# Optimization experiments

Measured on AMD Instinct MI355X. Metric: run time of the kernel, lower is better.

Reference implementation:

```python
import jax, jax.numpy as jnp
import numpy as np

HIDDEN = 4096
N_HEADS = 32
N_KV_HEADS = 8
HEAD_DIM = HIDDEN // N_HEADS  # 128
ROPE_THETA = 10000.0


def rotate_half(x):
    x1, x2 = jnp.split(x, 2, axis=-1)
    return jnp.concatenate((-x2, x1), axis=-1)


def rope_cos_sin(seq_len, dim, theta, dtype):
    inv_freq = 1.0 / (theta ** (jnp.arange(0, dim, 2, dtype=jnp.float32) / dim))
    t = jnp.arange(seq_len, dtype=jnp.float32)
    freqs = jnp.outer(t, inv_freq)               # [S, D/2]
    emb = jnp.concatenate((freqs, freqs), axis=-1)  # [S, D]
    return jnp.cos(emb).astype(dtype), jnp.sin(emb).astype(dtype)


def setup_inputs() -> dict:
    key = jax.random.key(0)
    k0, k1, k2, k3, k4 = jax.random.split(key, 5)
    B, S = 1, 2048
    std = 1.0 / np.sqrt(HIDDEN)
    return {
        "hidden_states": jax.random.normal(k0, (B, S, HIDDEN), dtype=jnp.float32),
        "wq": jax.random.normal(k1, (N_HEADS * HEAD_DIM, HIDDEN), dtype=jnp.float32) * std,
        "wk": jax.random.normal(k2, (N_KV_HEADS * HEAD_DIM, HIDDEN), dtype=jnp.float32) * std,
        "wv": jax.random.normal(k3, (N_KV_HEADS * HEAD_DIM, HIDDEN), dtype=jnp.float32) * std,
        "wo": jax.random.normal(k4, (HIDDEN, N_HEADS * HEAD_DIM), dtype=jnp.float32) * std,
    }


def reference(hidden_states, wq, wk, wv, wo):
    B, S, _ = hidden_states.shape
    dtype = hidden_states.dtype
    G = N_HEADS // N_KV_HEADS  # query groups per kv head

    # projections (torch Linear: x @ W.T)
    q = (hidden_states @ wq.T).reshape(B, S, N_HEADS, HEAD_DIM).transpose(0, 2, 1, 3)      # [B,H,S,D]
    k = (hidden_states @ wk.T).reshape(B, S, N_KV_HEADS, HEAD_DIM).transpose(0, 2, 1, 3)   # [B,Hkv,S,D]
    v = (hidden_states @ wv.T).reshape(B, S, N_KV_HEADS, HEAD_DIM).transpose(0, 2, 1, 3)   # [B,Hkv,S,D]

    cos, sin = rope_cos_sin(S, HEAD_DIM, ROPE_THETA, dtype)  # [S,D]
    cos = cos[None, None]  # [1,1,S,D]
    sin = sin[None, None]
    q = q * cos + rotate_half(q) * sin
    k = k * cos + rotate_half(k) * sin

    # GQA: group query heads with their kv head (equivalent to repeat_interleave on kv)
    qg = q.reshape(B, N_KV_HEADS, G, S, HEAD_DIM)
    scale = 1.0 / np.sqrt(HEAD_DIM)
    scores = jnp.einsum("bkgsd,bktd->bkgst", qg, k) * scale  # [B,Hkv,G,S,S]

    causal = jnp.tril(jnp.ones((S, S), dtype=bool))
    scores = jnp.where(causal, scores, -jnp.inf)
    probs = jax.nn.softmax(scores.astype(jnp.float32), axis=-1).astype(dtype)

    out = jnp.einsum("bkgst,bktd->bkgsd", probs, v)  # [B,Hkv,G,S,D]
    out = out.reshape(B, N_HEADS, S, HEAD_DIM).transpose(0, 2, 1, 3).reshape(B, S, N_HEADS * HEAD_DIM)
    return out @ wo.T
```

## Files before the change

kernel.cpp:

```cpp
#include <hip/hip_runtime.h>
#include <hip/hip_bf16.h>


typedef _Float16 half4_t __attribute__((ext_vector_type(4)));
typedef _Float16 half8_t __attribute__((ext_vector_type(8)));
typedef float f32x4 __attribute__((ext_vector_type(4)));

#define S_LEN 2048
#define HID 4096
#define NH 32
#define NKV 8

__device__ __forceinline__ void gload_lds16(const void* g, void* l) {
  __builtin_amdgcn_global_load_lds((const __attribute__((address_space(1))) void*)g,
                                   (__attribute__((address_space(3))) void*)l, 16, 0, 0);
}

__global__ __launch_bounds__(256) void cvt_f32_f16(const float* __restrict__ src,
                                                   _Float16* __restrict__ dst, int n4) {
  int i = blockIdx.x * 256 + threadIdx.x;
  if (i >= n4) return;
  f32x4 v = *(const f32x4*)(src + (size_t)i * 4);
  half4_t h = {(_Float16)v[0], (_Float16)v[1], (_Float16)v[2], (_Float16)v[3]};
  *(half4_t*)(dst + (size_t)i * 4) = h;
}

__global__ __launch_bounds__(256) void cvt_qkv(const float* __restrict__ wq,
                                               const float* __restrict__ wk,
                                               const float* __restrict__ wv,
                                               _Float16* __restrict__ dst, int n4) {
  int i = blockIdx.x * 256 + threadIdx.x;
  if (i >= n4) return;
  size_t e = (size_t)i * 4;
  const float* src;
  size_t off;
  if (e < (size_t)4096 * 4096)      { src = wq; off = e; }
  else if (e < (size_t)5120 * 4096) { src = wk; off = e - (size_t)4096 * 4096; }
  else                              { src = wv; off = e - (size_t)5120 * 4096; }
  f32x4 v = *(const f32x4*)(src + off);
  half4_t h = {(_Float16)v[0], (_Float16)v[1], (_Float16)v[2], (_Float16)v[3]};
  *(half4_t*)(dst + e) = h;
}

__global__ __launch_bounds__(256) void rope_table_kernel(float* __restrict__ cost,
                                                         float* __restrict__ sint) {
  int i = blockIdx.x * 256 + threadIdx.x;
  int d = i & 63;
  int s = i >> 6;
  float inv = exp2f(-(float)d * (13.287712379549449f / 64.0f));
  float f = (float)s * inv;
  cost[i] = cosf(f);
  sint[i] = sinf(f);
}

__global__ __launch_bounds__(256) void rope_apply_q(_Float16* __restrict__ X,
                                                    const float* __restrict__ cost,
                                                    const float* __restrict__ sint) {
  int idx = blockIdx.x * 256 + threadIdx.x;
  int g = idx & 15;
  int tmp = idx >> 4;
  int h = tmp % NH;
  int s = tmp / NH;
  int d0 = g * 4;
  size_t base = (size_t)s * HID + h * 128 + d0;
  half4_t x1 = *(half4_t*)(X + base);
  half4_t x2 = *(half4_t*)(X + base + 64);
  const float* cp = cost + s * 64 + d0;
  const float* sp = sint + s * 64 + d0;
  half4_t y1, y2;
#pragma unroll
  for (int j = 0; j < 4; ++j) {
    float c = cp[j], sn = sp[j];
    float a = (float)x1[j], b = (float)x2[j];
    y1[j] = (_Float16)(a * c - b * sn);
    y2[j] = (_Float16)(b * c + a * sn);
  }
  *(half4_t*)(X + base) = y1;
  *(half4_t*)(X + base + 64) = y2;
}

__global__ __launch_bounds__(256) void rope_k2_inplace(_Float16* __restrict__ K2,
                                                       const float* __restrict__ cost,
                                                       const float* __restrict__ sint) {
  int idx = blockIdx.x * 256 + threadIdx.x;
  int g = idx & 15;
  int tmp = idx >> 4;
  int h = tmp % NKV;
  int s = tmp / NKV;
  int d0 = g * 4;
  size_t tb = (size_t)h * (S_LEN * 128) + (size_t)(s >> 4) * 2048 + (size_t)(s & 15) * 8;
  size_t a1 = tb + (size_t)(d0 >> 3) * 128 + (d0 & 7);
  size_t a2 = a1 + 1024;
  half4_t x1 = *(half4_t*)(K2 + a1);
  half4_t x2 = *(half4_t*)(K2 + a2);
  const float* cp = cost + s * 64 + d0;
  const float* sp = sint + s * 64 + d0;
  half4_t y1, y2;
#pragma unroll
  for (int j = 0; j < 4; ++j) {
    float c = cp[j], sn = sp[j];
    float a = (float)x1[j], b = (float)x2[j];
    y1[j] = (_Float16)(a * c - b * sn);
    y2[j] = (_Float16)(b * c + a * sn);
  }
  *(half4_t*)(K2 + a1) = y1;
  *(half4_t*)(K2 + a2) = y2;
}

template <int MODE>
__global__ __launch_bounds__(256) void gemmT(const _Float16* __restrict__ A,
                                             const _Float16* __restrict__ W,
                                             void* __restrict__ out,
                                             _Float16* __restrict__ K2,
                                             _Float16* __restrict__ V2) {
  const int id = blockIdx.x;
  const int xcd = id & 7, slot = id >> 3;
  const int c = (MODE == 0) ? (xcd * 6 + (slot >> 4)) : (xcd * 4 + (slot >> 4));
  const int m0 = (slot & 15) * 128;
  const int col0 = c * 128;
  __shared__ __align__(16) _Float16 As[3][128 * 32];
  __shared__ __align__(16) _Float16 Bs[3][128 * 32];
  const int t = threadIdx.x, w = t >> 6, l = t & 63, lr = l & 15, lg = l >> 4;
  const int wm = (w >> 1) * 64, wn = (w & 1) * 64;
  const int srow = l >> 2;
  const int scolS = (((l & 3) ^ ((l >> 3) & 3))) * 8;
  const int rc = (lr >> 1) & 3;
  const _Float16* ap = A + (size_t)m0 * 4096 + scolS;
  const _Float16* bp = W + (size_t)col0 * 4096 + scolS;

  f32x4 acc[4][4] = {};

#define STAGE(buf_, kb_)                                              \
  _Pragma("unroll") for (int it = 0; it < 2; ++it) {                  \
    const int ci = it * 4 + w;                                        \
    const int r = ci * 16 + srow;                                     \
    gload_lds16(ap + (size_t)r * 4096 + (kb_), &As[buf_][ci * 512]);  \
    gload_lds16(bp + (size_t)r * 4096 + (kb_), &Bs[buf_][ci * 512]);  \
  }

  STAGE(0, 0)
  STAGE(1, 32)

  for (int k = 0; k < 128; ++k) {
    const int kb2 = (k + 2) * 32;
    const int buf = k % 3;
    __builtin_amdgcn_s_barrier();
    __builtin_amdgcn_sched_barrier(0);
    if (kb2 < 4096) {
      STAGE((k + 2) % 3, kb2)
      asm volatile("s_waitcnt vmcnt(4)" ::: "memory");
    } else {
      asm volatile("s_waitcnt vmcnt(0)" ::: "memory");
    }
    __builtin_amdgcn_sched_barrier(0);
    __builtin_amdgcn_s_barrier();
    half8_t af[4], bf[4];
#pragma unroll
    for (int mi = 0; mi < 4; ++mi)
      af[mi] = *(const half8_t*)&As[buf][(wm + mi * 16 + lr) * 32 + (lg ^ rc) * 8];
#pragma unroll
    for (int ni = 0; ni < 4; ++ni)
      bf[ni] = *(const half8_t*)&Bs[buf][(wn + ni * 16 + lr) * 32 + (lg ^ rc) * 8];
#pragma unroll
    for (int mi = 0; mi < 4; ++mi)
#pragma unroll
      for (int ni = 0; ni < 4; ++ni)
        acc[mi][ni] = __builtin_amdgcn_mfma_f32_16x16x32_f16(af[mi], bf[ni], acc[mi][ni], 0, 0, 0);
  }
#undef STAGE

#pragma unroll
  for (int mi = 0; mi < 4; ++mi) {
#pragma unroll
    for (int ni = 0; ni < 4; ++ni) {
      const int row = m0 + wm + mi * 16 + lg * 4;
      const int col = col0 + wn + ni * 16 + lr;
      if (MODE == 1) {
#pragma unroll
        for (int i = 0; i < 4; ++i)
          ((float*)out)[(size_t)(row + i) * 4096 + col] = acc[mi][ni][i];
      } else {
        if (col < 4096) {
#pragma unroll
          for (int i = 0; i < 4; ++i)
            ((_Float16*)out)[(size_t)(row + i) * 4096 + col] = (_Float16)acc[mi][ni][i];
        } else if (col < 5120) {
          const int cl = col - 4096;
          const int h = cl >> 7, d = cl & 127;
          const size_t kk = (size_t)h * (S_LEN * 128) + (size_t)(row >> 4) * 2048 +
                            (size_t)(d >> 3) * 128 + (d & 7);
#pragma unroll
          for (int i = 0; i < 4; ++i)
            K2[kk + ((row + i) & 15) * 8] = (_Float16)acc[mi][ni][i];
        } else {
          const int cl = col - 5120;
          half4_t o;
#pragma unroll
          for (int i = 0; i < 4; ++i) o[i] = (_Float16)acc[mi][ni][i];
          *(half4_t*)(V2 + (size_t)(cl >> 7) * (S_LEN * 128) + (size_t)(row >> 4) * 2048 +
                      (size_t)(cl & 127) * 16 + (row & 15)) = o;
        }
      }
    }
  }
}

__global__ __launch_bounds__(256) void attn_kernel(const _Float16* __restrict__ Q,
                                                   const _Float16* __restrict__ K2,
                                                   const _Float16* __restrict__ V2,
                                                   _Float16* __restrict__ Op,
                                                   float* __restrict__ Md) {
  const int bid = blockIdx.x;
  const int hk = bid & 7;
  const int split = (bid >> 3) & 1;
  const int qt = 63 - (bid >> 4);
  const int w = threadIdx.x >> 6;
  const int h = hk * 4 + w;
  const int l = threadIdx.x & 63;
  const int lr = l & 15;
  const int lg = l >> 4;
  const float scale = 0.08838834764831845f;
  const float LOG2E = 1.4426950408889634f;
  const float NEG = -1.0e30f;

  const int half_steps = qt + 1;
  const int kt0 = split * half_steps;
  const int kt1 = kt0 + half_steps;

  int sq[2];
  half8_t qf[2][4];
#pragma unroll
  for (int qc = 0; qc < 2; ++qc) {
    sq[qc] = qt * 32 + qc * 16 + lr;
#pragma unroll
    for (int c = 0; c < 4; ++c)
      qf[qc][c] = *(const half8_t*)(Q + (size_t)sq[qc] * HID + h * 128 + c * 32 + lg * 8);
  }
  const _Float16* Kb = K2 + (size_t)hk * (S_LEN * 128);
  const _Float16* Vb = V2 + (size_t)hk * (S_LEN * 128);

  f32x4 acc[8][2] = {};
  float m[2] = {NEG, NEG};
  float den[2] = {0.f, 0.f};

  half8_t kfn[4];
#pragma unroll
  for (int c = 0; c < 4; ++c)
    kfn[c] = *(const half8_t*)(Kb + (size_t)kt0 * 2048 + (c * 4 + lg) * 128 + lr * 8);

  for (int kt = kt0; kt < kt1; ++kt) {
    half8_t kf[4];
#pragma unroll
    for (int c = 0; c < 4; ++c) kf[c] = kfn[c];
    if (kt + 1 < kt1) {
#pragma unroll
      for (int c = 0; c < 4; ++c)
        kfn[c] = *(const half8_t*)(Kb + (size_t)(kt + 1) * 2048 + (c * 4 + lg) * 128 + lr * 8);
    }
    f32x4 s0 = {0.f, 0.f, 0.f, 0.f}, s1 = {0.f, 0.f, 0.f, 0.f};
    __builtin_amdgcn_s_setprio(1);
#pragma unroll
    for (int c = 0; c < 4; ++c) {
      s0 = __builtin_amdgcn_mfma_f32_16x16x32_f16(kf[c], qf[0][c], s0, 0, 0, 0);
      s1 = __builtin_amdgcn_mfma_f32_16x16x32_f16(kf[c], qf[1][c], s1, 0, 0, 0);
    }
    __builtin_amdgcn_s_setprio(0);
    half4_t vf[8];
#pragma unroll
    for (int dc = 0; dc < 8; ++dc)
      vf[dc] = *(const half4_t*)(Vb + (size_t)kt * 2048 + (dc * 16 + lr) * 16 + lg * 4);
    const int kbase = kt * 16 + lg * 4;
    float sc[2][4];
#pragma unroll
    for (int i = 0; i < 4; ++i) {
      sc[0][i] = s0[i] * scale;
      sc[1][i] = s1[i] * scale;
    }
    if (kt >= 2 * qt) {
#pragma unroll
      for (int qc = 0; qc < 2; ++qc)
#pragma unroll
        for (int i = 0; i < 4; ++i)
          if (kbase + i > sq[qc]) sc[qc][i] = NEG;
    }
    half4_t pf[2];
#pragma unroll
    for (int qc = 0; qc < 2; ++qc) {
      float mx = fmaxf(fmaxf(sc[qc][0], sc[qc][1]), fmaxf(sc[qc][2], sc[qc][3]));
      mx = fmaxf(mx, __shfl_xor(mx, 16));
      mx = fmaxf(mx, __shfl_xor(mx, 32));
      if (!__all(mx - m[qc] <= 8.0f)) {
        float mn = fmaxf(m[qc], mx);
        float corr = exp2f((m[qc] - mn) * LOG2E);
        den[qc] *= corr;
#pragma unroll
        for (int dc = 0; dc < 8; ++dc)
#pragma unroll
          for (int i = 0; i < 4; ++i) acc[dc][qc][i] *= corr;
        m[qc] = mn;
      }
      float ps = 0.f, p[4];
#pragma unroll
      for (int i = 0; i < 4; ++i) {
        p[i] = exp2f((sc[qc][i] - m[qc]) * LOG2E);
        ps += p[i];
      }
      ps += __shfl_xor(ps, 16);
      ps += __shfl_xor(ps, 32);
      den[qc] += ps;
      pf[qc] = (half4_t){(_Float16)p[0], (_Float16)p[1], (_Float16)p[2], (_Float16)p[3]};
    }
    __builtin_amdgcn_s_setprio(1);
#pragma unroll
    for (int dc = 0; dc < 8; ++dc) {
      acc[dc][0] = __builtin_amdgcn_mfma_f32_16x16x16f16(vf[dc], pf[0], acc[dc][0], 0, 0, 0);
      acc[dc][1] = __builtin_amdgcn_mfma_f32_16x16x16f16(vf[dc], pf[1], acc[dc][1], 0, 0, 0);
    }
    __builtin_amdgcn_s_setprio(0);
  }

  _Float16* Os = Op + (size_t)split * S_LEN * HID;
#pragma unroll
  for (int qc = 0; qc < 2; ++qc) {
    float inv = den[qc] > 0.f ? 1.0f / den[qc] : 0.f;
#pragma unroll
    for (int dc = 0; dc < 8; ++dc) {
      half4_t o;
#pragma unroll
      for (int i = 0; i < 4; ++i) o[i] = (_Float16)(acc[dc][qc][i] * inv);
      *(half4_t*)(Os + (size_t)sq[qc] * HID + h * 128 + dc * 16 + lg * 4) = o;
    }
    if (lg == 0) {
      int mdix = ((split * S_LEN + sq[qc]) * NH + h) * 2;
      Md[mdix] = m[qc];
      Md[mdix + 1] = den[qc];
    }
  }
}

__global__ __launch_bounds__(256) void attn_combine(const _Float16* __restrict__ Op,
                                                    const float* __restrict__ Md,
                                                    _Float16* __restrict__ O) {
  const float LOG2E = 1.4426950408889634f;
  int idx = blockIdx.x * 256 + threadIdx.x;
  int dd = (idx & 15) * 8;
  int h = (idx >> 4) & 31;
  int s = idx >> 9;
  int base = (s * NH + h) * 2;
  float m0 = Md[base], den0 = Md[base + 1];
  float m1 = Md[S_LEN * NH * 2 + base], den1 = Md[S_LEN * NH * 2 + base + 1];
  float M = fmaxf(m0, m1);
  float w0 = den0 * exp2f((m0 - M) * LOG2E);
  float w1 = den1 * exp2f((m1 - M) * LOG2E);
  float r = 1.0f / (w0 + w1);
  w0 *= r;
  w1 *= r;
  size_t off = (size_t)s * HID + h * 128 + dd;
  half8_t a = *(const half8_t*)(Op + off);
  half8_t b = *(const half8_t*)(Op + (size_t)S_LEN * HID + off);
  half8_t o;
#pragma unroll
  for (int j = 0; j < 8; ++j) o[j] = (_Float16)(w0 * (float)a[j] + w1 * (float)b[j]);
  *(half8_t*)(O + off) = o;
}

extern "C" void kernel_launch(void* const* d_in, const int* in_sizes, int n_in,
                              void* d_out, int out_size, void* d_ws, size_t ws_size,
                              hipStream_t stream) {
  (void)in_sizes; (void)n_in; (void)out_size; (void)ws_size;
  const float* hs = (const float*)d_in[0];
  const float* wq = (const float*)d_in[1];
  const float* wk = (const float*)d_in[2];
  const float* wv = (const float*)d_in[3];
  const float* wo = (const float*)d_in[4];

  char* ws = (char*)d_ws;
  _Float16* hs_h = (_Float16*)(ws);
  _Float16* q_h  = (_Float16*)(ws + (16u << 20));
  _Float16* K2   = (_Float16*)(ws + (32u << 20));
  _Float16* V2   = (_Float16*)(ws + (36u << 20));
  float* cost    = (float*)(ws + (40u << 20));
  float* sint    = (float*)(ws + (40u << 20) + (512u << 10));
  _Float16* wqkv = (_Float16*)(ws + (41u << 20));
  _Float16* Op   = wqkv;
  float* Md      = (float*)(ws + (73u << 20));
  _Float16* wo_h = wqkv;
  _Float16* o_h  = hs_h;

  cvt_f32_f16<<<8192, 256, 0, stream>>>(hs, hs_h, (S_LEN * HID) / 4);
  rope_table_kernel<<<(S_LEN * 64) / 256, 256, 0, stream>>>(cost, sint);
  cvt_qkv<<<24576, 256, 0, stream>>>(wq, wk, wv, wqkv, (6144 * 4096) / 4);

  gemmT<0><<<768, 256, 0, stream>>>(hs_h, wqkv, q_h, K2, V2);

  rope_apply_q<<<(S_LEN * NH * 16) / 256, 256, 0, stream>>>(q_h, cost, sint);
  rope_k2_inplace<<<(S_LEN * NKV * 16) / 256, 256, 0, stream>>>(K2, cost, sint);

  attn_kernel<<<1024, 256, 0, stream>>>(q_h, K2, V2, Op, Md);
  attn_combine<<<4096, 256, 0, stream>>>(Op, Md, o_h);

  cvt_f32_f16<<<16384, 256, 0, stream>>>(wo, wo_h, (HID * HID) / 4);
  gemmT<1><<<512, 256, 0, stream>>>(o_h, wo_h, d_out, nullptr, nullptr);
}
```

Measured before the change: 379.3 us.

## Halve attention query tile to 16 rows per wave and double grid

The attention kernel now gives each wave a single 16-row query chunk instead of two, so the grid doubles to 2048 blocks and the KV range is split evenly between two halves. The goal is more blocks and waves to fill the GPU, fewer registers per thread for higher occupancy, and finer causal load balance. In exchange each K/V tile loaded from global memory feeds only one score MFMA chain rather than two, so K/V traffic per unit of work doubles and data reuse drops.

```diff
diff --git a/kernel.cpp b/kernel.cpp
--- a/kernel.cpp
+++ b/kernel.cpp
@@ -213,7 +213,7 @@
   const int bid = blockIdx.x;
   const int hk = bid & 7;
   const int split = (bid >> 3) & 1;
-  const int qt = 63 - (bid >> 4);
+  const int qt = 127 - (bid >> 4);
   const int w = threadIdx.x >> 6;
   const int h = hk * 4 + w;
   const int l = threadIdx.x & 63;
@@ -223,118 +223,100 @@
   const float LOG2E = 1.4426950408889634f;
   const float NEG = -1.0e30f;
 
-  const int half_steps = qt + 1;
-  const int kt0 = split * half_steps;
-  const int kt1 = kt0 + half_steps;
-
-  int sq[2];
-  half8_t qf[2][4];
-#pragma unroll
-  for (int qc = 0; qc < 2; ++qc) {
-    sq[qc] = qt * 32 + qc * 16 + lr;
-#pragma unroll
-    for (int c = 0; c < 4; ++c)
-      qf[qc][c] = *(const half8_t*)(Q + (size_t)sq[qc] * HID + h * 128 + c * 32 + lg * 8);
-  }
+  const int nkt = qt + 1;
+  const int h0 = (nkt + 1) >> 1;
+  const int kt0 = split ? h0 : 0;
+  const int kt1 = split ? nkt : h0;
+  const int sq = qt * 16 + lr;
+
+  half8_t qf[4];
+#pragma unroll
+  for (int c = 0; c < 4; ++c)
+    qf[c] = *(const half8_t*)(Q + (size_t)sq * HID + h * 128 + c * 32 + lg * 8);
   const _Float16* Kb = K2 + (size_t)hk * (S_LEN * 128);
   const _Float16* Vb = V2 + (size_t)hk * (S_LEN * 128);
 
-  f32x4 acc[8][2] = {};
-  float m[2] = {NEG, NEG};
-  float den[2] = {0.f, 0.f};
-
-  half8_t kfn[4];
-#pragma unroll
-  for (int c = 0; c < 4; ++c)
-    kfn[c] = *(const half8_t*)(Kb + (size_t)kt0 * 2048 + (c * 4 + lg) * 128 + lr * 8);
-
-  for (int kt = kt0; kt < kt1; ++kt) {
-    half8_t kf[4];
-#pragma unroll
-    for (int c = 0; c < 4; ++c) kf[c] = kfn[c];
-    if (kt + 1 < kt1) {
+  f32x4 acc[8] = {};
+  float m = NEG, den = 0.f;
+
+  if (kt0 < kt1) {
+    half8_t kfn[4];
+#pragma unroll
+    for (int c = 0; c < 4; ++c)
+      kfn[c] = *(const half8_t*)(Kb + (size_t)kt0 * 2048 + (c * 4 + lg) * 128 + lr * 8);
+
+    for (int kt = kt0; kt < kt1; ++kt) {
+      half8_t kf[4];
+#pragma unroll
+      for (int c = 0; c < 4; ++c) kf[c] = kfn[c];
+      if (kt + 1 < kt1) {
+#pragma unroll
+        for (int c = 0; c < 4; ++c)
+          kfn[c] = *(const half8_t*)(Kb + (size_t)(kt + 1) * 2048 + (c * 4 + lg) * 128 + lr * 8);
+      }
+      f32x4 s0 = {0.f, 0.f, 0.f, 0.f};
+      __builtin_amdgcn_s_setprio(1);
 #pragma unroll
       for (int c = 0; c < 4; ++c)
-        kfn[c] = *(const half8_t*)(Kb + (size_t)(kt + 1) * 2048 + (c * 4 + lg) * 128 + lr * 8);
-    }
-    f32x4 s0 = {0.f, 0.f, 0.f, 0.f}, s1 = {0.f, 0.f, 0.f, 0.f};
-    __builtin_amdgcn_s_setprio(1);
-#pragma unroll
-    for (int c = 0; c < 4; ++c) {
-      s0 = __builtin_amdgcn_mfma_f32_16x16x32_f16(kf[c], qf[0][c], s0, 0, 0, 0);
-      s1 = __builtin_amdgcn_mfma_f32_16x16x32_f16(kf[c], qf[1][c], s1, 0, 0, 0);
-    }
-    __builtin_amdgcn_s_setprio(0);
-    half4_t vf[8];
-#pragma unroll
-    for (int dc = 0; dc < 8; ++dc)
-      vf[dc] = *(const half4_t*)(Vb + (size_t)kt * 2048 + (dc * 16 + lr) * 16 + lg * 4);
-    const int kbase = kt * 16 + lg * 4;
-    float sc[2][4];
-#pragma unroll
-    for (int i = 0; i < 4; ++i) {
-      sc[0][i] = s0[i] * scale;
-      sc[1][i] = s1[i] * scale;
-    }
-    if (kt >= 2 * qt) {
-#pragma unroll
-      for (int qc = 0; qc < 2; ++qc)
+        s0 = __builtin_amdgcn_mfma_f32_16x16x32_f16(kf[c], qf[c], s0, 0, 0, 0);
+      __builtin_amdgcn_s_setprio(0);
+      half4_t vf[8];
+#pragma unroll
+      for (int dc = 0; dc < 8; ++dc)
+        vf[dc] = *(const half4_t*)(Vb + (size_t)kt * 2048 + (dc * 16 + lr) * 16 + lg * 4);
+      const int kbase = kt * 16 + lg * 4;
+      float sc[4];
+#pragma unroll
+      for (int i = 0; i < 4; ++i) sc[i] = s0[i] * scale;
+      if (kt == qt) {
 #pragma unroll
         for (int i = 0; i < 4; ++i)
-          if (kbase + i > sq[qc]) sc[qc][i] = NEG;
-    }
-    half4_t pf[2];
-#pragma unroll
-    for (int qc = 0; qc < 2; ++qc) {
-      float mx = fmaxf(fmaxf(sc[qc][0], sc[qc][1]), fmaxf(sc[qc][2], sc[qc][3]));
+          if (kbase + i > sq) sc[i] = NEG;
+      }
+      float mx = fmaxf(fmaxf(sc[0], sc[1]), fmaxf(sc[2], sc[3]));
       mx = fmaxf(mx, __shfl_xor(mx, 16));
       mx = fmaxf(mx, __shfl_xor(mx, 32));
-      if (!__all(mx - m[qc] <= 8.0f)) {
-        float mn = fmaxf(m[qc], mx);
-        float corr = exp2f((m[qc] - mn) * LOG2E);
-        den[qc] *= corr;
+      if (!__all(mx - m <= 8.0f)) {
+        float mn = fmaxf(m, mx);
+        float corr = exp2f((m - mn) * LOG2E);
+        den *= corr;
 #pragma unroll
         for (int dc = 0; dc < 8; ++dc)
 #pragma unroll
-          for (int i = 0; i < 4; ++i) acc[dc][qc][i] *= corr;
-        m[qc] = mn;
+          for (int i = 0; i < 4; ++i) acc[dc][i] *= corr;
+        m = mn;
       }
       float ps = 0.f, p[4];
 #pragma unroll
       for (int i = 0; i < 4; ++i) {
-        p[i] = exp2f((sc[qc][i] - m[qc]) * LOG2E);
+        p[i] = exp2f((sc[i] - m) * LOG2E);
         ps += p[i];
       }
       ps += __shfl_xor(ps, 16);
       ps += __shfl_xor(ps, 32);
-      den[qc] += ps;
-      pf[qc] = (half4_t){(_Float16)p[0], (_Float16)p[1], (_Float16)p[2], (_Float16)p[3]};
+      den += ps;
+      half4_t pf = {(_Float16)p[0], (_Float16)p[1], (_Float16)p[2], (_Float16)p[3]};
+      __builtin_amdgcn_s_setprio(1);
+#pragma unroll
+      for (int dc = 0; dc < 8; ++dc)
+        acc[dc] = __builtin_amdgcn_mfma_f32_16x16x16f16(vf[dc], pf, acc[dc], 0, 0, 0);
+      __builtin_amdgcn_s_setprio(0);
     }
-    __builtin_amdgcn_s_setprio(1);
-#pragma unroll
-    for (int dc = 0; dc < 8; ++dc) {
-      acc[dc][0] = __builtin_amdgcn_mfma_f32_16x16x16f16(vf[dc], pf[0], acc[dc][0], 0, 0, 0);
-      acc[dc][1] = __builtin_amdgcn_mfma_f32_16x16x16f16(vf[dc], pf[1], acc[dc][1], 0, 0, 0);
-    }
-    __builtin_amdgcn_s_setprio(0);
   }
 
   _Float16* Os = Op + (size_t)split * S_LEN * HID;
-#pragma unroll
-  for (int qc = 0; qc < 2; ++qc) {
-    float inv = den[qc] > 0.f ? 1.0f / den[qc] : 0.f;
-#pragma unroll
-    for (int dc = 0; dc < 8; ++dc) {
-      half4_t o;
-#pragma unroll
-      for (int i = 0; i < 4; ++i) o[i] = (_Float16)(acc[dc][qc][i] * inv);
-      *(half4_t*)(Os + (size_t)sq[qc] * HID + h * 128 + dc * 16 + lg * 4) = o;
-    }
-    if (lg == 0) {
-      int mdix = ((split * S_LEN + sq[qc]) * NH + h) * 2;
-      Md[mdix] = m[qc];
-      Md[mdix + 1] = den[qc];
-    }
+  const float inv = den > 0.f ? 1.0f / den : 0.f;
+#pragma unroll
+  for (int dc = 0; dc < 8; ++dc) {
+    half4_t o;
+#pragma unroll
+    for (int i = 0; i < 4; ++i) o[i] = (_Float16)(acc[dc][i] * inv);
+    *(half4_t*)(Os + (size_t)sq * HID + h * 128 + dc * 16 + lg * 4) = o;
+  }
+  if (lg == 0) {
+    int mdix = ((split * S_LEN + sq) * NH + h) * 2;
+    Md[mdix] = m;
+    Md[mdix + 1] = den;
   }
 }
 
@@ -396,7 +378,7 @@
   rope_apply_q<<<(S_LEN * NH * 16) / 256, 256, 0, stream>>>(q_h, cost, sint);
   rope_k2_inplace<<<(S_LEN * NKV * 16) / 256, 256, 0, stream>>>(K2, cost, sint);
 
-  attn_kernel<<<1024, 256, 0, stream>>>(q_h, K2, V2, Op, Md);
+  attn_kernel<<<2048, 256, 0, stream>>>(q_h, K2, V2, Op, Md);
   attn_combine<<<4096, 256, 0, stream>>>(Op, Md, o_h);
 
   cvt_f32_f16<<<16384, 256, 0, stream>>>(wo, wo_h, (HID * HID) / 4);
```

Result: slower. 416.7 us (+9.9%).
